# Kernel optimization log

Hardware: AMD Instinct MI355X
Metric: run time of the kernel (lower is better)

The kernel has to match this reference:

```python
import jax, jax.numpy as jnp
import numpy as np

DIM = 1024
HEADS = 8
NUM_EXPERTS = 65536
NUM_KEYS = 256  # sqrt(NUM_EXPERTS)
DIM_KEY = 512
TOPK = 16  # product_key_topk == num_experts_per_head


def setup_inputs() -> dict:
    key = jax.random.key(0)
    ks = jax.random.split(key, 6)
    B, N = 2, 512
    x = jax.random.normal(ks[0], (B, N, DIM), dtype=jnp.float32)
    gamma = jnp.ones((DIM,), dtype=jnp.float32)
    wq = jax.random.normal(ks[1], (2 * HEADS * DIM_KEY, DIM), dtype=jnp.float32) * 0.02
    keys = jax.random.normal(ks[2], (HEADS, NUM_KEYS, 2, DIM_KEY), dtype=jnp.float32) * 0.02
    table_down = jax.random.normal(ks[3], (NUM_EXPERTS, DIM), dtype=jnp.float32) * 0.02
    table_up = jax.random.normal(ks[4], (NUM_EXPERTS, DIM), dtype=jnp.float32) * 0.02
    return {"x": x, "gamma": gamma, "wq": wq, "keys": keys,
            "table_down": table_down, "table_up": table_up}


def _rmsnorm(v, g):
    # torch F.normalize(x, dim=-1) * gamma * sqrt(dim)
    scale = jnp.sqrt(jnp.asarray(v.shape[-1], v.dtype))
    n = jnp.maximum(jnp.linalg.norm(v, axis=-1, keepdims=True), 1e-12)
    return v / n * g * scale


def reference(x, gamma, wq, keys, table_down, table_up):
    B, N, D = x.shape
    xn = _rmsnorm(x, gamma)          # pre_rmsnorm on x
    gate = xn                        # x_in_gate is None -> gate = norm(x)
    # queries: b n (p h d) -> p b n h d
    q = gate @ wq.T                  # [B,N,2*H*DK]
    q = q.reshape(B, N, 2, HEADS, DIM_KEY).transpose(2, 0, 1, 3, 4)  # [2,B,N,H,DK]
    # sim: p b n h d, h k p d -> p b n h k
    sim = jnp.einsum('pbnhd,hkpd->pbnhk', q, keys)
    sx, ix = jax.lax.top_k(sim[0], TOPK)  # [B,N,H,TOPK]
    sy, iy = jax.lax.top_k(sim[1], TOPK)
    # outer sums over the two product-key axes -> [B,N,H,TOPK*TOPK]
    all_scores = (sx[..., :, None] + sy[..., None, :]).reshape(B, N, HEADS, TOPK * TOPK)
    all_indices = (ix[..., :, None] * NUM_KEYS + iy[..., None, :]).reshape(B, N, HEADS, TOPK * TOPK)
    scores, pk = jax.lax.top_k(all_scores, TOPK)           # [B,N,H,K]
    indices = jnp.take_along_axis(all_indices, pk, axis=-1)  # expert ids [B,N,H,K]
    wd = table_down[indices]  # [B,N,H,K,D]
    wu = table_up[indices]    # [B,N,H,K,D]
    h = jnp.einsum('bnd,bnhkd->bnhk', xn, wd)
    h = jax.nn.gelu(h, approximate=False) * jax.nn.softmax(scores, axis=-1)
    out = jnp.einsum('bnhk,bnhkd->bnd', h, wu)
    return out
```

## Files before the change

kernel.cpp:

```cpp
#include <hip/hip_runtime.h>
#include <math.h>


#define DIMV 1024

__global__ __launch_bounds__(256) void peer_rmsnorm(const float* __restrict__ x,
                                                    const float* __restrict__ gamma,
                                                    float* __restrict__ xnf)
{
    int t = blockIdx.x;
    int tid = threadIdx.x;
    const float4* xr = (const float4*)(x + (size_t)t * DIMV);
    float4 v = xr[tid];
    double ss = (double)v.x*v.x + (double)v.y*v.y + (double)v.z*v.z + (double)v.w*v.w;
    #pragma unroll
    for (int off = 32; off > 0; off >>= 1) ss += __shfl_xor(ss, off);
    __shared__ double red[4];
    if ((tid & 63) == 0) red[tid >> 6] = ss;
    __syncthreads();
    double tot = red[0] + red[1] + red[2] + red[3];
    float n32 = (float)fmax(sqrt(tot), 1e-12);
    const float4* g4 = (const float4*)gamma;
    float4 gv = g4[tid];
    float4 o;
    o.x = __fmul_rn(__fmul_rn(__fdiv_rn(v.x, n32), gv.x), 32.0f);
    o.y = __fmul_rn(__fmul_rn(__fdiv_rn(v.y, n32), gv.y), 32.0f);
    o.z = __fmul_rn(__fmul_rn(__fdiv_rn(v.z, n32), gv.z), 32.0f);
    o.w = __fmul_rn(__fmul_rn(__fdiv_rn(v.w, n32), gv.w), 32.0f);
    ((float4*)(xnf + (size_t)t * DIMV))[tid] = o;
}

__global__ __launch_bounds__(256) void peer_qgemm(const float* __restrict__ A,
                                                  const float* __restrict__ Bm,
                                                  float* __restrict__ C)
{
    __shared__ float As[2][8][128];
    __shared__ float Bs[2][8][128];
    int tid = threadIdx.x;
    int m0 = blockIdx.y * 128, n0 = blockIdx.x * 128;
    int tx = tid & 15, ty = tid >> 4;
    int lrow = tid >> 1, lk = (tid & 1) * 4;
    float acc[8][8] = {};
    float4 av = *(const float4*)(A  + (long)(m0 + lrow) * 1024 + lk);
    float4 bv = *(const float4*)(Bm + (long)(n0 + lrow) * 1024 + lk);
    #pragma unroll
    for (int j = 0; j < 4; j++) {
        As[0][lk + j][lrow] = ((const float*)&av)[j];
        Bs[0][lk + j][lrow] = ((const float*)&bv)[j];
    }
    __syncthreads();
    int cur = 0;
    for (int k0 = 0; k0 < 1024; k0 += 8) {
        bool more = (k0 + 8) < 1024;
        if (more) {
            av = *(const float4*)(A  + (long)(m0 + lrow) * 1024 + (k0 + 8 + lk));
            bv = *(const float4*)(Bm + (long)(n0 + lrow) * 1024 + (k0 + 8 + lk));
        }
        #pragma unroll
        for (int kk = 0; kk < 8; kk++) {
            float4 a0 = *(const float4*)&As[cur][kk][ty * 8];
            float4 a1 = *(const float4*)&As[cur][kk][ty * 8 + 4];
            float4 b0 = *(const float4*)&Bs[cur][kk][tx * 4];
            float4 b1 = *(const float4*)&Bs[cur][kk][tx * 4 + 64];
            float ra8[8] = {a0.x,a0.y,a0.z,a0.w,a1.x,a1.y,a1.z,a1.w};
            float rb8[8] = {b0.x,b0.y,b0.z,b0.w,b1.x,b1.y,b1.z,b1.w};
            #pragma unroll
            for (int i = 0; i < 8; i++)
                #pragma unroll
                for (int j = 0; j < 8; j++)
                    acc[i][j] = __fmaf_rn(ra8[i], rb8[j], acc[i][j]);
        }
        if (more) {
            int nxt = cur ^ 1;
            #pragma unroll
            for (int j = 0; j < 4; j++) {
                As[nxt][lk + j][lrow] = ((const float*)&av)[j];
                Bs[nxt][lk + j][lrow] = ((const float*)&bv)[j];
            }
            __syncthreads();
            cur = nxt;
        }
    }
    #pragma unroll
    for (int i = 0; i < 8; i++) {
        float4 c0 = {acc[i][0], acc[i][1], acc[i][2], acc[i][3]};
        float4 c1 = {acc[i][4], acc[i][5], acc[i][6], acc[i][7]};
        long r = (long)(m0 + ty * 8 + i) * 8192 + n0;
        *(float4*)(C + r + tx * 4)      = c0;
        *(float4*)(C + r + 64 + tx * 4) = c1;
    }
}

__global__ __launch_bounds__(256) void peer_sim(const float* __restrict__ qf,
                                                const float* __restrict__ keys,
                                                float* __restrict__ simf)
{
    int tb = blockIdx.x;
    int z  = blockIdx.y;
    int h = z & 7, p = z >> 3;
    int tid = threadIdx.x;
    __shared__ float4 qs[16][128];
    int t0 = tb * 16;
    long qbase = (long)h * 512 + (long)p * 4096;
    int row = tid >> 4, c0 = (tid & 15) * 8;
    const float4* qrow = (const float4*)(qf + (long)(t0 + row) * 8192 + qbase);
    #pragma unroll
    for (int u = 0; u < 8; u++) qs[row][c0 + u] = qrow[c0 + u];
    __syncthreads();
    int k = tid;
    const float4* krow = (const float4*)(keys + (long)h * 262144 + (long)k * 1024 + (long)p * 512);
    float pa[16][4] = {};
    for (int d4 = 0; d4 < 128; d4++) {
        float4 kv = krow[d4];
        #pragma unroll
        for (int tt = 0; tt < 16; tt++) {
            float4 qv = qs[tt][d4];
            pa[tt][0] = __fadd_rn(pa[tt][0], __fmul_rn(qv.x, kv.x));
            pa[tt][1] = __fadd_rn(pa[tt][1], __fmul_rn(qv.y, kv.y));
            pa[tt][2] = __fadd_rn(pa[tt][2], __fmul_rn(qv.z, kv.z));
            pa[tt][3] = __fadd_rn(pa[tt][3], __fmul_rn(qv.w, kv.w));
        }
    }
    #pragma unroll
    for (int tt = 0; tt < 16; tt++) {
        float s = __fadd_rn(__fadd_rn(pa[tt][0], pa[tt][2]),
                            __fadd_rn(pa[tt][1], pa[tt][3]));
        simf[(long)(t0 + tt) * 4096 + (long)p * 2048 + h * 256 + k] = s;
    }
}

__device__ inline void peer_select16(float v[4], int lane, float* outv, int* outi)
{
    for (int iter = 0; iter < 16; iter++) {
        float bv = -INFINITY; int bk = 1 << 30;
        #pragma unroll
        for (int i = 0; i < 4; i++) {
            int k = i * 64 + lane;
            if (v[i] > bv || (v[i] == bv && k < bk)) { bv = v[i]; bk = k; }
        }
        #pragma unroll
        for (int off = 32; off > 0; off >>= 1) {
            float ov = __shfl_xor(bv, off);
            int   ok = __shfl_xor(bk, off);
            if (ov > bv || (ov == bv && ok < bk)) { bv = ov; bk = ok; }
        }
        if (lane == 0) { outv[iter] = bv; outi[iter] = bk; }
        __syncthreads();
        if ((bk & 63) == lane) v[bk >> 6] = -INFINITY;
    }
}

__global__ __launch_bounds__(64) void peer_topk(const float* __restrict__ sim,
                                                float* __restrict__ wsel,
                                                int* __restrict__ esel)
{
    int b = blockIdx.x;
    int t = b >> 3, h = b & 7;
    int lane = threadIdx.x;
    const float* simx = sim + (size_t)t * 4096 + h * 256;
    const float* simy = simx + 2048;
    __shared__ float sxv[16]; __shared__ int sxi[16];
    __shared__ float syv[16]; __shared__ int syi[16];
    __shared__ float cv[16];  __shared__ int cf[16];
    float v[4];
    #pragma unroll
    for (int i = 0; i < 4; i++) v[i] = simx[i*64 + lane];
    peer_select16(v, lane, sxv, sxi);
    __syncthreads();
    #pragma unroll
    for (int i = 0; i < 4; i++) v[i] = simy[i*64 + lane];
    peer_select16(v, lane, syv, syi);
    __syncthreads();
    #pragma unroll
    for (int i = 0; i < 4; i++) {
        int f = i*64 + lane;
        v[i] = __fadd_rn(sxv[f >> 4], syv[f & 15]);
    }
    peer_select16(v, lane, cv, cf);
    __syncthreads();
    double m = (double)cv[0];
    double w = (lane < 16) ? exp((double)cv[lane] - m) : 0.0;
    double Z = w;
    #pragma unroll
    for (int off = 32; off > 0; off >>= 1) Z += __shfl_xor(Z, off);
    if (lane < 16) {
        int f = cf[lane];
        esel[b * 16 + lane] = sxi[f >> 4] * 256 + syi[f & 15];
        wsel[b * 16 + lane] = (float)(w / Z);
    }
}

__global__ __launch_bounds__(256) void peer_down(const float* __restrict__ xn,
                                                 const float* __restrict__ table_down,
                                                 const int* __restrict__ esel,
                                                 const float* __restrict__ wsel,
                                                 float* __restrict__ g)
{
    int tid = threadIdx.x;
    int wv = (blockIdx.x << 2) | (tid >> 6);
    int lane = tid & 63;
    int t = wv >> 7;
    __shared__ float4 xs[256];
    xs[tid] = ((const float4*)(xn + (size_t)t * DIMV))[tid];
    __syncthreads();
    int e = esel[wv];
    const float4* dr = (const float4*)(table_down + (size_t)e * DIMV);
    double acc = 0.0;
    #pragma unroll
    for (int it = 0; it < 4; it++) {
        int d4 = it * 64 + lane;
        float4 a = xs[d4];
        float4 bb = dr[d4];
        acc = fma((double)a.x, (double)bb.x, acc);
        acc = fma((double)a.y, (double)bb.y, acc);
        acc = fma((double)a.z, (double)bb.z, acc);
        acc = fma((double)a.w, (double)bb.w, acc);
    }
    #pragma unroll
    for (int off = 32; off > 0; off >>= 1) acc += __shfl_xor(acc, off);
    if (lane == 0) {
        double hv = acc;
        double ge = 0.5 * hv * (1.0 + erf(hv * 0.70710678118654752));
        g[wv] = (float)(ge * (double)wsel[wv]);
    }
}

__global__ __launch_bounds__(64) void peer_up(const float* __restrict__ table_up,
                                              const int* __restrict__ esel,
                                              const float* __restrict__ gbuf,
                                              float* __restrict__ out)
{
    int t  = blockIdx.x >> 2;
    int ds = blockIdx.x & 3;
    int lane = threadIdx.x;
    __shared__ float gs[128];
    __shared__ int   es[128];
    gs[lane]      = gbuf[t * 128 + lane];
    gs[lane + 64] = gbuf[t * 128 + 64 + lane];
    es[lane]      = esel[t * 128 + lane];
    es[lane + 64] = esel[t * 128 + 64 + lane];
    __syncthreads();
    int dbase = ds * 256 + lane * 4;
    double a0 = 0, a1 = 0, a2 = 0, a3 = 0;
    for (int j = 0; j < 128; j++) {
        const float4 u = *(const float4*)(table_up + (size_t)es[j] * DIMV + dbase);
        double gj = (double)gs[j];
        a0 = fma(gj, (double)u.x, a0); a1 = fma(gj, (double)u.y, a1);
        a2 = fma(gj, (double)u.z, a2); a3 = fma(gj, (double)u.w, a3);
    }
    float4 o = {(float)a0, (float)a1, (float)a2, (float)a3};
    *(float4*)(out + (size_t)t * DIMV + dbase) = o;
}

extern "C" void kernel_launch(void* const* d_in, const int* in_sizes, int n_in,
                              void* d_out, int out_size, void* d_ws, size_t ws_size,
                              hipStream_t stream)
{
    const float* x          = (const float*)d_in[0];
    const float* gamma      = (const float*)d_in[1];
    const float* wq         = (const float*)d_in[2];
    const float* keys       = (const float*)d_in[3];
    const float* table_down = (const float*)d_in[4];
    const float* table_up   = (const float*)d_in[5];
    float* out = (float*)d_out;
    char* wsb  = (char*)d_ws;

    float* xnf  = (float*)(wsb);
    float* qf   = (float*)(wsb + (4ull<<20));
    float* simf = (float*)(wsb + (36ull<<20));
    float* wsel = (float*)(wsb + (52ull<<20));
    int*   esel = (int*)  (wsb + (52ull<<20) + (512ull<<10));
    float* g    = (float*)(wsb + (53ull<<20));
    if (ws_size < (54ull << 20)) return;

    peer_rmsnorm<<<1024, 256, 0, stream>>>(x, gamma, xnf);

    peer_qgemm<<<dim3(64, 8, 1), 256, 0, stream>>>(xnf, wq, qf);

    peer_sim<<<dim3(64, 16, 1), 256, 0, stream>>>(qf, keys, simf);

    peer_topk<<<8192, 64, 0, stream>>>(simf, wsel, esel);

    peer_down<<<32768, 256, 0, stream>>>(xnf, table_down, esel, wsel, g);

    peer_up<<<4096, 64, 0, stream>>>(table_up, esel, g, out);
}
```

Measured before the change: 557.3 us.

## Fuse expert down and up projections per token; widen GEMM k-tile to 16

The separate down-projection kernel (one wave per expert) and up-projection kernel are merged into one kernel with a block per token. Each of the four waves computes 32 expert dot products into shared memory, then all threads accumulate the up projection. This removes a launch and the round trip of the gate buffer through global memory. It also cuts the grid from 32768 plus 4096 blocks to 1024, which may lower memory-level parallelism for the random table gathers. Separately, the query GEMM's k-tile is doubled from 8 to 16, halving the number of barriers per block at the cost of more shared memory.

Result: faster. 543.0 us (-2.6%).

```diff
diff --git a/kernel.cpp b/kernel.cpp
--- a/kernel.cpp
+++ b/kernel.cpp
@@ -34,30 +34,36 @@
                                                   const float* __restrict__ Bm,
                                                   float* __restrict__ C)
 {
-    __shared__ float As[2][8][128];
-    __shared__ float Bs[2][8][128];
+    __shared__ float As[2][16][128];
+    __shared__ float Bs[2][16][128];
     int tid = threadIdx.x;
     int m0 = blockIdx.y * 128, n0 = blockIdx.x * 128;
     int tx = tid & 15, ty = tid >> 4;
-    int lrow = tid >> 1, lk = (tid & 1) * 4;
+    int lrow = tid >> 1, lk8 = (tid & 1) * 8;
     float acc[8][8] = {};
-    float4 av = *(const float4*)(A  + (long)(m0 + lrow) * 1024 + lk);
-    float4 bv = *(const float4*)(Bm + (long)(n0 + lrow) * 1024 + lk);
+    float4 av0 = *(const float4*)(A  + (long)(m0 + lrow) * 1024 + lk8);
+    float4 av1 = *(const float4*)(A  + (long)(m0 + lrow) * 1024 + lk8 + 4);
+    float4 bv0 = *(const float4*)(Bm + (long)(n0 + lrow) * 1024 + lk8);
+    float4 bv1 = *(const float4*)(Bm + (long)(n0 + lrow) * 1024 + lk8 + 4);
     #pragma unroll
     for (int j = 0; j < 4; j++) {
-        As[0][lk + j][lrow] = ((const float*)&av)[j];
-        Bs[0][lk + j][lrow] = ((const float*)&bv)[j];
+        As[0][lk8 + j][lrow]     = ((const float*)&av0)[j];
+        As[0][lk8 + 4 + j][lrow] = ((const float*)&av1)[j];
+        Bs[0][lk8 + j][lrow]     = ((const float*)&bv0)[j];
+        Bs[0][lk8 + 4 + j][lrow] = ((const float*)&bv1)[j];
     }
     __syncthreads();
     int cur = 0;
-    for (int k0 = 0; k0 < 1024; k0 += 8) {
-        bool more = (k0 + 8) < 1024;
+    for (int k0 = 0; k0 < 1024; k0 += 16) {
+        bool more = (k0 + 16) < 1024;
         if (more) {
-            av = *(const float4*)(A  + (long)(m0 + lrow) * 1024 + (k0 + 8 + lk));
-            bv = *(const float4*)(Bm + (long)(n0 + lrow) * 1024 + (k0 + 8 + lk));
-        }
-        #pragma unroll
-        for (int kk = 0; kk < 8; kk++) {
+            av0 = *(const float4*)(A  + (long)(m0 + lrow) * 1024 + (k0 + 16 + lk8));
+            av1 = *(const float4*)(A  + (long)(m0 + lrow) * 1024 + (k0 + 16 + lk8 + 4));
+            bv0 = *(const float4*)(Bm + (long)(n0 + lrow) * 1024 + (k0 + 16 + lk8));
+            bv1 = *(const float4*)(Bm + (long)(n0 + lrow) * 1024 + (k0 + 16 + lk8 + 4));
+        }
+        #pragma unroll
+        for (int kk = 0; kk < 16; kk++) {
             float4 a0 = *(const float4*)&As[cur][kk][ty * 8];
             float4 a1 = *(const float4*)&As[cur][kk][ty * 8 + 4];
             float4 b0 = *(const float4*)&Bs[cur][kk][tx * 4];
@@ -74,8 +80,10 @@
             int nxt = cur ^ 1;
             #pragma unroll
             for (int j = 0; j < 4; j++) {
-                As[nxt][lk + j][lrow] = ((const float*)&av)[j];
-                Bs[nxt][lk + j][lrow] = ((const float*)&bv)[j];
+                As[nxt][lk8 + j][lrow]     = ((const float*)&av0)[j];
+                As[nxt][lk8 + 4 + j][lrow] = ((const float*)&av1)[j];
+                Bs[nxt][lk8 + j][lrow]     = ((const float*)&bv0)[j];
+                Bs[nxt][lk8 + 4 + j][lrow] = ((const float*)&bv1)[j];
             }
             __syncthreads();
             cur = nxt;
@@ -190,58 +198,49 @@
     }
 }
 
-__global__ __launch_bounds__(256) void peer_down(const float* __restrict__ xn,
-                                                 const float* __restrict__ table_down,
-                                                 const int* __restrict__ esel,
-                                                 const float* __restrict__ wsel,
-                                                 float* __restrict__ g)
-{
-    int tid = threadIdx.x;
-    int wv = (blockIdx.x << 2) | (tid >> 6);
-    int lane = tid & 63;
-    int t = wv >> 7;
+__global__ __launch_bounds__(256) void peer_downup(const float* __restrict__ xn,
+                                                   const float* __restrict__ table_down,
+                                                   const float* __restrict__ table_up,
+                                                   const int* __restrict__ esel,
+                                                   const float* __restrict__ wsel,
+                                                   float* __restrict__ out)
+{
+    int t = blockIdx.x;
+    int tid = threadIdx.x;
+    int wid = tid >> 6, lane = tid & 63;
     __shared__ float4 xs[256];
+    __shared__ float  gs[128];
+    __shared__ int    es[128];
+    if (tid < 128) es[tid] = esel[t * 128 + tid];
     xs[tid] = ((const float4*)(xn + (size_t)t * DIMV))[tid];
     __syncthreads();
-    int e = esel[wv];
-    const float4* dr = (const float4*)(table_down + (size_t)e * DIMV);
-    double acc = 0.0;
-    #pragma unroll
-    for (int it = 0; it < 4; it++) {
-        int d4 = it * 64 + lane;
-        float4 a = xs[d4];
-        float4 bb = dr[d4];
-        acc = fma((double)a.x, (double)bb.x, acc);
-        acc = fma((double)a.y, (double)bb.y, acc);
-        acc = fma((double)a.z, (double)bb.z, acc);
-        acc = fma((double)a.w, (double)bb.w, acc);
-    }
-    #pragma unroll
-    for (int off = 32; off > 0; off >>= 1) acc += __shfl_xor(acc, off);
-    if (lane == 0) {
-        double hv = acc;
-        double ge = 0.5 * hv * (1.0 + erf(hv * 0.70710678118654752));
-        g[wv] = (float)(ge * (double)wsel[wv]);
-    }
-}
-
-__global__ __launch_bounds__(64) void peer_up(const float* __restrict__ table_up,
-                                              const int* __restrict__ esel,
-                                              const float* __restrict__ gbuf,
-                                              float* __restrict__ out)
-{
-    int t  = blockIdx.x >> 2;
-    int ds = blockIdx.x & 3;
-    int lane = threadIdx.x;
-    __shared__ float gs[128];
-    __shared__ int   es[128];
-    gs[lane]      = gbuf[t * 128 + lane];
-    gs[lane + 64] = gbuf[t * 128 + 64 + lane];
-    es[lane]      = esel[t * 128 + lane];
-    es[lane + 64] = esel[t * 128 + 64 + lane];
-    __syncthreads();
-    int dbase = ds * 256 + lane * 4;
+    #pragma unroll 2
+    for (int jj = 0; jj < 32; jj++) {
+        int j = wid * 32 + jj;
+        const float4* dr = (const float4*)(table_down + (size_t)es[j] * DIMV);
+        double acc = 0.0;
+        #pragma unroll
+        for (int it = 0; it < 4; it++) {
+            int d4 = it * 64 + lane;
+            float4 a = xs[d4];
+            float4 bb = dr[d4];
+            acc = fma((double)a.x, (double)bb.x, acc);
+            acc = fma((double)a.y, (double)bb.y, acc);
+            acc = fma((double)a.z, (double)bb.z, acc);
+            acc = fma((double)a.w, (double)bb.w, acc);
+        }
+        #pragma unroll
+        for (int off = 32; off > 0; off >>= 1) acc += __shfl_xor(acc, off);
+        if (lane == 0) {
+            double hv = acc;
+            double ge = 0.5 * hv * (1.0 + erf(hv * 0.70710678118654752));
+            gs[j] = (float)(ge * (double)wsel[t * 128 + j]);
+        }
+    }
+    __syncthreads();
+    int dbase = tid * 4;
     double a0 = 0, a1 = 0, a2 = 0, a3 = 0;
+    #pragma unroll 4
     for (int j = 0; j < 128; j++) {
         const float4 u = *(const float4*)(table_up + (size_t)es[j] * DIMV + dbase);
         double gj = (double)gs[j];
@@ -270,7 +269,6 @@
     float* simf = (float*)(wsb + (36ull<<20));
     float* wsel = (float*)(wsb + (52ull<<20));
     int*   esel = (int*)  (wsb + (52ull<<20) + (512ull<<10));
-    float* g    = (float*)(wsb + (53ull<<20));
     if (ws_size < (54ull << 20)) return;
 
     peer_rmsnorm<<<1024, 256, 0, stream>>>(x, gamma, xnf);
@@ -281,7 +279,6 @@
 
     peer_topk<<<8192, 64, 0, stream>>>(simf, wsel, esel);
 
-    peer_down<<<32768, 256, 0, stream>>>(xnf, table_down, esel, wsel, g);
-
-    peer_up<<<4096, 64, 0, stream>>>(table_up, esel, g, out);
-}
+    peer_downup<<<1024, 256, 0, stream>>>(xnf, table_down, table_up,
+                                          esel, wsel, out);
+}
```
